# Kernel tuning notes

Measured on AMD Instinct MI355X. Metric: run time of the kernel, lower is better.

## Reference

```python
import jax, jax.numpy as jnp
import numpy as np

B, FRAMES, NBINS, HOP = 4, 400, 129, 240
T = FRAMES * HOP  # 96000


def hann_window(K, dtype=jnp.float32):
    # torch.hann_window default is periodic=True: 0.5*(1 - cos(2*pi*n/K))
    n = jnp.arange(K, dtype=dtype)
    return 0.5 - 0.5 * jnp.cos(2.0 * jnp.pi * n / K)


def get_minimum_phase_fir(log_mag):
    # log_mag: [B, F, NBINS] -> full spectrum [B, F, N], N = 2*(NBINS-1)
    full = jnp.concatenate([log_mag, jnp.flip(log_mag, -1)[..., 1:-1]], axis=-1)
    N = full.shape[-1]
    # Hilbert transform (scipy-style analytic signal), N even
    Xf = jnp.fft.fft(full, axis=-1)
    h = jnp.concatenate([
        jnp.ones((1,), full.dtype),
        2.0 * jnp.ones((N // 2 - 1,), full.dtype),
        jnp.ones((1,), full.dtype),
        jnp.zeros((N // 2 - 1,), full.dtype),
    ])
    analytic = jnp.fft.ifft(Xf * h, axis=-1)
    min_phase = -jnp.imag(analytic)
    freq_resp = jnp.exp(full + 1j * min_phase)
    return jnp.real(jnp.fft.ifft(freq_resp, axis=-1))  # [B, F, N]


def windowing(kernel):
    K = kernel.shape[-1]
    w = hann_window(K, kernel.dtype)
    w = w.at[: K // 2].set(1.0)
    return kernel * w


def upsample_linear(x, scale):
    # x: [B, K, L] -> [B, K, L*scale], matches F.upsample(mode='linear', align_corners=False)
    L = x.shape[-1]
    out = jnp.arange(L * scale, dtype=x.dtype)
    src = jnp.clip((out + 0.5) / scale - 0.5, 0.0, L - 1.0)
    lo = jnp.floor(src).astype(jnp.int32)
    hi = jnp.minimum(lo + 1, L - 1)
    w = src - lo.astype(x.dtype)
    return x[..., lo] * (1.0 - w) + x[..., hi] * w


def fir_filt(x, h):
    # x: [B, T], h: [B, T, K]; causal time-varying FIR: y[t] = sum_k h[t,k] * x[t-k]
    K = h.shape[-1]
    Tn = x.shape[-1]
    x_pad = jnp.pad(x, ((0, 0), (K - 1, 0)))
    idx = jnp.arange(Tn)[:, None] + jnp.arange(K)[None, :]  # [T, K]
    frames = x_pad[:, idx]  # [B, T, K] (im2col-like gather)
    return jnp.einsum('btk,btk->bt', frames, jnp.flip(h, -1))


def setup_inputs() -> dict:
    key = jax.random.key(0)
    k1, k2 = jax.random.split(key)
    ex = jax.random.normal(k1, (B, T), dtype=jnp.float32)
    log_mag = jax.random.normal(k2, (B, FRAMES, NBINS), dtype=jnp.float32)
    return {"ex": ex, "log_mag": log_mag, "hop_length": HOP}


def reference(ex, log_mag, hop_length):
    kernel = get_minimum_phase_fir(log_mag)          # [B, F, K]
    kernel = windowing(kernel)
    up = upsample_linear(jnp.transpose(kernel, (0, 2, 1)), hop_length)  # [B, K, F*hop]
    up = jnp.transpose(up, (0, 2, 1))                # [B, F*hop, K]
    Tn = min(ex.shape[1], up.shape[1])
    ex = ex[:, :Tn]
    up = up[:, :Tn]
    return fir_filt(ex, up)
```

## Files before the change

kernel.cpp:

```cpp
#include <hip/hip_runtime.h>
#include <math.h>

#define NB 4
#define FRAMES 400
#define NBINS 129
#define HOP 240
#define T_LEN (FRAMES * HOP)
#define KLEN 256

#define REC_C { const float cn_ = fmaf(a2, cm, -cm1); cm1 = cm; cm = cn_; }
#define REC_S { const float sn_ = fmaf(a2, sm, -sm1); sm1 = sm; sm = sn_; }

__global__ __launch_bounds__(256) void gen_fir(const float* __restrict__ log_mag,
                                               float* __restrict__ kern) {
    const int bf  = blockIdx.x;
    const int tid = threadIdx.x;
    const int n   = tid & 127;
    const int h   = tid >> 7;

    __shared__ __align__(16) float  full[132];
    __shared__ __align__(16) float  pg[2][128];
    __shared__ __align__(16) float  pm[2][128];
    __shared__ __align__(16) float2 crci[128];
    __shared__ __align__(16) float  pe[2][128];
    __shared__ __align__(16) float  po[2][128];

    const float* lm = log_mag + bf * NBINS;
    if (tid < NBINS) full[tid] = lm[tid];

    const float rev_n = (float)n * (1.0f / 256.0f);
    const float ca = __builtin_amdgcn_cosf(rev_n);
    const float sa = __builtin_amdgcn_sinf(rev_n);
    const float a2  = 2.0f * ca;
    const float sgn = (n & 1) ? -1.0f : 1.0f;

    float cm0, cm1_0, sm0, sm1_0;
    if (h == 0) {
        cm0 = 1.0f;  cm1_0 = ca;
        sm0 = 0.0f;  sm1_0 = -sa;
    } else {
        const float r64 = (float)((64 * n) & 255) * (1.0f / 256.0f);
        const float r63 = (float)((63 * n) & 255) * (1.0f / 256.0f);
        cm0   = __builtin_amdgcn_cosf(r64);
        sm0   = __builtin_amdgcn_sinf(r64);
        cm1_0 = __builtin_amdgcn_cosf(r63);
        sm1_0 = __builtin_amdgcn_sinf(r63);
    }
    __syncthreads();

    const float full0   = full[0];
    const float full128 = full[128];

    {
        const float4* f4p = (const float4*)full;
        float cm1 = cm1_0, cm = cm0, acc = 0.0f;
#pragma unroll 8
        for (int u = 16 * h; u < 16 * h + 16; ++u) {
            const float4 f4 = f4p[u];
            acc = fmaf(f4.x, cm, acc); REC_C;
            acc = fmaf(f4.y, cm, acc); REC_C;
            acc = fmaf(f4.z, cm, acc); REC_C;
            acc = fmaf(f4.w, cm, acc); REC_C;
        }
        const float share = h ? (sgn * full128) : (-full0);
        pg[h][n] = acc * (1.0f / 64.0f) + share * (1.0f / 128.0f);
    }
    __syncthreads();

    {
        const float4* p0 = (const float4*)pg[0];
        const float4* p1 = (const float4*)pg[1];
        float sm1 = sm1_0, sm = sm0, acc = 0.0f;
#pragma unroll 8
        for (int u = 16 * h; u < 16 * h + 16; ++u) {
            const float4 a4 = p0[u];
            const float4 b4 = p1[u];
            acc = fmaf(a4.x + b4.x, sm, acc); REC_S;
            acc = fmaf(a4.y + b4.y, sm, acc); REC_S;
            acc = fmaf(a4.z + b4.z, sm, acc); REC_S;
            acc = fmaf(a4.w + b4.w, sm, acc); REC_S;
        }
        pm[h][n] = acc;
    }
    __syncthreads();

    if (h == 0) {
        const float mp = -(pm[0][n] + pm[1][n]);
        const float e  = __builtin_amdgcn_exp2f(full[n] * 1.4426950408889634f);
        float rev = mp * 0.15915494309189535f;
        rev = rev - floorf(rev);
        const float smp  = __builtin_amdgcn_sinf(rev);
        const float cmp_ = __builtin_amdgcn_cosf(rev);
        const float sc = (n == 0) ? 1.0f : 2.0f;
        crci[n] = make_float2(sc * e * cmp_, sc * e * smp);
    }
    __syncthreads();

    {
        const float4* cc4 = (const float4*)crci;
        float cm1 = cm1_0, cm = cm0;
        float sm1 = sm1_0, sm = sm0;
        float accE = 0.0f, accO = 0.0f;
#pragma unroll 8
        for (int u = 32 * h; u < 32 * h + 32; ++u) {
            const float4 q = cc4[u];
            accE = fmaf(q.x, cm, accE); accE = fmaf(-q.y, sm, accE);
            REC_C; REC_S;
            accO = fmaf(q.z, cm, accO); accO = fmaf(-q.w, sm, accO);
            REC_C; REC_S;
        }
        pe[h][n] = accE;
        po[h][n] = accO;
    }
    __syncthreads();

    if (h == 0) {
        const float accE = pe[0][n] + pe[1][n];
        const float accO = po[0][n] + po[1][n];
        const float e128 = __builtin_amdgcn_exp2f(full128 * 1.4426950408889634f);
        const float base = sgn * e128;
        const float s = 1.0f / 256.0f;
        kern[bf * KLEN + n]       = (accE + accO + base) * s;
        kern[bf * KLEN + n + 128] = (accE - accO + base) * s * (0.5f + 0.5f * ca);
    }
}

__global__ __launch_bounds__(256) void fir_apply(const float* __restrict__ ex,
                                                 const float* __restrict__ kern,
                                                 float* __restrict__ out) {
    const int b   = blockIdx.y;
    const int t0  = blockIdx.x * 512;
    const int tid = threadIdx.x;

    __shared__ __align__(16) float  xs[768];
    __shared__ __align__(16) float2 kp[4][258];

    for (int i = tid; i < 768; i += 256) {
        const int t = t0 - 255 + i;
        xs[i] = (t >= 0 && t < T_LEN) ? ex[b * T_LEN + t] : 0.0f;
    }

    float src0 = ((float)t0 + 0.5f) * (1.0f / HOP) - 0.5f;
    src0 = fminf(fmaxf(src0, 0.0f), (float)(FRAMES - 1));
    const int f0 = (int)src0;
    const float* kb = kern + b * FRAMES * KLEN;
    for (int i = tid; i < 4 * KLEN; i += 256) {
        const int q = i >> 8;
        const int j = i & 255;
        const int fl = min(f0 + q,     FRAMES - 1);
        const int fh = min(f0 + q + 1, FRAMES - 1);
        kp[q][j] = make_float2(kb[fl * KLEN + j], kb[fh * KLEN + j]);
    }
    __syncthreads();

    const int te = t0 + 2 * tid;
    float se = ((float)te + 0.5f) * (1.0f / HOP) - 0.5f;
    se = fminf(fmaxf(se, 0.0f), (float)(FRAMES - 1));
    float so = ((float)te + 1.5f) * (1.0f / HOP) - 0.5f;
    so = fminf(fmaxf(so, 0.0f), (float)(FRAMES - 1));
    const int   lo = (int)se;
    const float we = se - (float)lo;
    const float wo = so - (float)lo;

    const float4* kq4 = (const float4*)&kp[lo - f0][0];

    const int base = 2 * tid;
    float carry = xs[base + 256];
    float aeL = 0.0f, aeH = 0.0f, aoL = 0.0f, aoH = 0.0f;
#pragma unroll 8
    for (int u = 0; u < 128; ++u) {
        const float2 v  = *(const float2*)&xs[base + 254 - 2 * u];
        const float4 k4 = kq4[u];
        aeL = fmaf(v.y,   k4.x, aeL);  aeH = fmaf(v.y,   k4.y, aeH);
        aoL = fmaf(carry, k4.x, aoL);  aoH = fmaf(carry, k4.y, aoH);
        aeL = fmaf(v.x,   k4.z, aeL);  aeH = fmaf(v.x,   k4.w, aeH);
        aoL = fmaf(v.y,   k4.z, aoL);  aoH = fmaf(v.y,   k4.w, aoH);
        carry = v.x;
    }

    if (te < T_LEN)     out[b * T_LEN + te]     = (1.0f - we) * aeL + we * aeH;
    if (te + 1 < T_LEN) out[b * T_LEN + te + 1] = (1.0f - wo) * aoL + wo * aoH;
}

extern "C" void kernel_launch(void* const* d_in, const int* in_sizes, int n_in,
                              void* d_out, int out_size, void* d_ws, size_t ws_size,
                              hipStream_t stream) {
    const float* ex      = (const float*)d_in[0];
    const float* log_mag = (const float*)d_in[1];
    float* kern = (float*)d_ws;
    float* out  = (float*)d_out;

    gen_fir<<<NB * FRAMES, 256, 0, stream>>>(log_mag, kern);

    dim3 grid((T_LEN + 511) / 512, NB);
    fir_apply<<<grid, 256, 0, stream>>>(ex, kern, out);
}
```

Baseline: 24.31 us.

## Fuse FIR generation and filtering into one kernel with per-frame ready flags

Merges the two launches into one grid. The first blocks compute per-frame minimum-phase FIRs and publish a per-row flag. The remaining blocks spin on the flags for the frames they need before loading kernels and filtering. This aims to remove the inter-kernel launch gap and tail, and to overlap filter work with FIR generation. It adds a memset launch, spin-wait overhead, and a forward-progress dependency on generator blocks being scheduled before the consumers that wait on them.

```diff
diff --git a/kernel.cpp b/kernel.cpp
--- a/kernel.cpp
+++ b/kernel.cpp
@@ -7,133 +7,147 @@
 #define HOP 240
 #define T_LEN (FRAMES * HOP)
 #define KLEN 256
+#define NGEN (NB * FRAMES)
+#define NFIRX 188
+#define NFIR (NFIRX * NB)
 
 #define REC_C { const float cn_ = fmaf(a2, cm, -cm1); cm1 = cm; cm = cn_; }
 #define REC_S { const float sn_ = fmaf(a2, sm, -sm1); sm1 = sm; sm = sn_; }
 
-__global__ __launch_bounds__(256) void gen_fir(const float* __restrict__ log_mag,
-                                               float* __restrict__ kern) {
-    const int bf  = blockIdx.x;
+__global__ __launch_bounds__(256) void ltv_fused(const float* __restrict__ ex,
+                                                 const float* __restrict__ log_mag,
+                                                 float* __restrict__ kern,
+                                                 int* __restrict__ flags,
+                                                 float* __restrict__ out) {
+    const int bid = blockIdx.x;
     const int tid = threadIdx.x;
-    const int n   = tid & 127;
-    const int h   = tid >> 7;
-
-    __shared__ __align__(16) float  full[132];
-    __shared__ __align__(16) float  pg[2][128];
-    __shared__ __align__(16) float  pm[2][128];
-    __shared__ __align__(16) float2 crci[128];
-    __shared__ __align__(16) float  pe[2][128];
-    __shared__ __align__(16) float  po[2][128];
-
-    const float* lm = log_mag + bf * NBINS;
-    if (tid < NBINS) full[tid] = lm[tid];
-
-    const float rev_n = (float)n * (1.0f / 256.0f);
-    const float ca = __builtin_amdgcn_cosf(rev_n);
-    const float sa = __builtin_amdgcn_sinf(rev_n);
-    const float a2  = 2.0f * ca;
-    const float sgn = (n & 1) ? -1.0f : 1.0f;
-
-    float cm0, cm1_0, sm0, sm1_0;
-    if (h == 0) {
-        cm0 = 1.0f;  cm1_0 = ca;
-        sm0 = 0.0f;  sm1_0 = -sa;
-    } else {
-        const float r64 = (float)((64 * n) & 255) * (1.0f / 256.0f);
-        const float r63 = (float)((63 * n) & 255) * (1.0f / 256.0f);
-        cm0   = __builtin_amdgcn_cosf(r64);
-        sm0   = __builtin_amdgcn_sinf(r64);
-        cm1_0 = __builtin_amdgcn_cosf(r63);
-        sm1_0 = __builtin_amdgcn_sinf(r63);
-    }
-    __syncthreads();
-
-    const float full0   = full[0];
-    const float full128 = full[128];
-
-    {
-        const float4* f4p = (const float4*)full;
-        float cm1 = cm1_0, cm = cm0, acc = 0.0f;
-#pragma unroll 8
-        for (int u = 16 * h; u < 16 * h + 16; ++u) {
-            const float4 f4 = f4p[u];
-            acc = fmaf(f4.x, cm, acc); REC_C;
-            acc = fmaf(f4.y, cm, acc); REC_C;
-            acc = fmaf(f4.z, cm, acc); REC_C;
-            acc = fmaf(f4.w, cm, acc); REC_C;
-        }
-        const float share = h ? (sgn * full128) : (-full0);
-        pg[h][n] = acc * (1.0f / 64.0f) + share * (1.0f / 128.0f);
-    }
-    __syncthreads();
-
-    {
-        const float4* p0 = (const float4*)pg[0];
-        const float4* p1 = (const float4*)pg[1];
-        float sm1 = sm1_0, sm = sm0, acc = 0.0f;
-#pragma unroll 8
-        for (int u = 16 * h; u < 16 * h + 16; ++u) {
-            const float4 a4 = p0[u];
-            const float4 b4 = p1[u];
-            acc = fmaf(a4.x + b4.x, sm, acc); REC_S;
-            acc = fmaf(a4.y + b4.y, sm, acc); REC_S;
-            acc = fmaf(a4.z + b4.z, sm, acc); REC_S;
-            acc = fmaf(a4.w + b4.w, sm, acc); REC_S;
-        }
-        pm[h][n] = acc;
-    }
-    __syncthreads();
-
-    if (h == 0) {
-        const float mp = -(pm[0][n] + pm[1][n]);
-        const float e  = __builtin_amdgcn_exp2f(full[n] * 1.4426950408889634f);
-        float rev = mp * 0.15915494309189535f;
-        rev = rev - floorf(rev);
-        const float smp  = __builtin_amdgcn_sinf(rev);
-        const float cmp_ = __builtin_amdgcn_cosf(rev);
-        const float sc = (n == 0) ? 1.0f : 2.0f;
-        crci[n] = make_float2(sc * e * cmp_, sc * e * smp);
-    }
-    __syncthreads();
-
-    {
-        const float4* cc4 = (const float4*)crci;
-        float cm1 = cm1_0, cm = cm0;
-        float sm1 = sm1_0, sm = sm0;
-        float accE = 0.0f, accO = 0.0f;
-#pragma unroll 8
-        for (int u = 32 * h; u < 32 * h + 32; ++u) {
-            const float4 q = cc4[u];
-            accE = fmaf(q.x, cm, accE); accE = fmaf(-q.y, sm, accE);
-            REC_C; REC_S;
-            accO = fmaf(q.z, cm, accO); accO = fmaf(-q.w, sm, accO);
-            REC_C; REC_S;
-        }
-        pe[h][n] = accE;
-        po[h][n] = accO;
-    }
-    __syncthreads();
-
-    if (h == 0) {
-        const float accE = pe[0][n] + pe[1][n];
-        const float accO = po[0][n] + po[1][n];
-        const float e128 = __builtin_amdgcn_exp2f(full128 * 1.4426950408889634f);
-        const float base = sgn * e128;
-        const float s = 1.0f / 256.0f;
-        kern[bf * KLEN + n]       = (accE + accO + base) * s;
-        kern[bf * KLEN + n + 128] = (accE - accO + base) * s * (0.5f + 0.5f * ca);
-    }
-}
-
-__global__ __launch_bounds__(256) void fir_apply(const float* __restrict__ ex,
-                                                 const float* __restrict__ kern,
-                                                 float* __restrict__ out) {
-    const int b   = blockIdx.y;
-    const int t0  = blockIdx.x * 512;
-    const int tid = threadIdx.x;
-
-    __shared__ __align__(16) float  xs[768];
-    __shared__ __align__(16) float2 kp[4][258];
+
+    __shared__ __align__(16) float smem[2832];
+
+    if (bid < NGEN) {
+        const int bf = bid;
+        const int n  = tid & 127;
+        const int h  = tid >> 7;
+
+        float*  full = smem;
+        float*  pg0  = smem + 136;
+        float*  pm0  = smem + 392;
+        float2* crci = (float2*)(smem + 648);
+        float*  pe0  = smem + 904;
+        float*  po0  = smem + 1160;
+
+        const float* lm = log_mag + bf * NBINS;
+        if (tid < NBINS) full[tid] = lm[tid];
+
+        const float rev_n = (float)n * (1.0f / 256.0f);
+        const float ca = __builtin_amdgcn_cosf(rev_n);
+        const float sa = __builtin_amdgcn_sinf(rev_n);
+        const float a2  = 2.0f * ca;
+        const float sgn = (n & 1) ? -1.0f : 1.0f;
+
+        float cm0, cm1_0, sm0, sm1_0;
+        if (h == 0) {
+            cm0 = 1.0f;  cm1_0 = ca;
+            sm0 = 0.0f;  sm1_0 = -sa;
+        } else {
+            const float r64 = (float)((64 * n) & 255) * (1.0f / 256.0f);
+            const float r63 = (float)((63 * n) & 255) * (1.0f / 256.0f);
+            cm0   = __builtin_amdgcn_cosf(r64);
+            sm0   = __builtin_amdgcn_sinf(r64);
+            cm1_0 = __builtin_amdgcn_cosf(r63);
+            sm1_0 = __builtin_amdgcn_sinf(r63);
+        }
+        __syncthreads();
+
+        const float full0   = full[0];
+        const float full128 = full[128];
+
+        {
+            const float4* f4p = (const float4*)full;
+            float cm1 = cm1_0, cm = cm0, acc = 0.0f;
+#pragma unroll 8
+            for (int u = 16 * h; u < 16 * h + 16; ++u) {
+                const float4 f4 = f4p[u];
+                acc = fmaf(f4.x, cm, acc); REC_C;
+                acc = fmaf(f4.y, cm, acc); REC_C;
+                acc = fmaf(f4.z, cm, acc); REC_C;
+                acc = fmaf(f4.w, cm, acc); REC_C;
+            }
+            const float share = h ? (sgn * full128) : (-full0);
+            pg0[h * 128 + n] = acc * (1.0f / 64.0f) + share * (1.0f / 128.0f);
+        }
+        __syncthreads();
+
+        {
+            const float4* p0 = (const float4*)pg0;
+            const float4* p1 = (const float4*)(pg0 + 128);
+            float sm1 = sm1_0, sm = sm0, acc = 0.0f;
+#pragma unroll 8
+            for (int u = 16 * h; u < 16 * h + 16; ++u) {
+                const float4 a4 = p0[u];
+                const float4 b4 = p1[u];
+                acc = fmaf(a4.x + b4.x, sm, acc); REC_S;
+                acc = fmaf(a4.y + b4.y, sm, acc); REC_S;
+                acc = fmaf(a4.z + b4.z, sm, acc); REC_S;
+                acc = fmaf(a4.w + b4.w, sm, acc); REC_S;
+            }
+            pm0[h * 128 + n] = acc;
+        }
+        __syncthreads();
+
+        if (h == 0) {
+            const float mp = -(pm0[n] + pm0[128 + n]);
+            const float e  = __builtin_amdgcn_exp2f(full[n] * 1.4426950408889634f);
+            float rev = mp * 0.15915494309189535f;
+            rev = rev - floorf(rev);
+            const float smp  = __builtin_amdgcn_sinf(rev);
+            const float cmp_ = __builtin_amdgcn_cosf(rev);
+            const float sc = (n == 0) ? 1.0f : 2.0f;
+            crci[n] = make_float2(sc * e * cmp_, sc * e * smp);
+        }
+        __syncthreads();
+
+        {
+            const float4* cc4 = (const float4*)crci;
+            float cm1 = cm1_0, cm = cm0;
+            float sm1 = sm1_0, sm = sm0;
+            float accE = 0.0f, accO = 0.0f;
+#pragma unroll 8
+            for (int u = 32 * h; u < 32 * h + 32; ++u) {
+                const float4 q = cc4[u];
+                accE = fmaf(q.x, cm, accE); accE = fmaf(-q.y, sm, accE);
+                REC_C; REC_S;
+                accO = fmaf(q.z, cm, accO); accO = fmaf(-q.w, sm, accO);
+                REC_C; REC_S;
+            }
+            pe0[h * 128 + n] = accE;
+            po0[h * 128 + n] = accO;
+        }
+        __syncthreads();
+
+        if (h == 0) {
+            const float accE = pe0[n] + pe0[128 + n];
+            const float accO = po0[n] + po0[128 + n];
+            const float e128 = __builtin_amdgcn_exp2f(full128 * 1.4426950408889634f);
+            const float base = sgn * e128;
+            const float s = 1.0f / 256.0f;
+            kern[bf * KLEN + n]       = (accE + accO + base) * s;
+            kern[bf * KLEN + n + 128] = (accE - accO + base) * s * (0.5f + 0.5f * ca);
+        }
+        __syncthreads();
+        if (tid == 0) {
+            __threadfence();
+            __hip_atomic_store(&flags[bf], 1, __ATOMIC_RELAXED, __HIP_MEMORY_SCOPE_AGENT);
+        }
+        return;
+    }
+
+    const int idx = bid - NGEN;
+    const int b   = idx / NFIRX;
+    const int t0  = (idx % NFIRX) * 512;
+
+    float*  xs = smem;
+    float2* kp = (float2*)(smem + 768);
 
     for (int i = tid; i < 768; i += 256) {
         const int t = t0 - 255 + i;
@@ -143,13 +157,26 @@
     float src0 = ((float)t0 + 0.5f) * (1.0f / HOP) - 0.5f;
     src0 = fminf(fmaxf(src0, 0.0f), (float)(FRAMES - 1));
     const int f0 = (int)src0;
+
+    if (tid == 0) {
+#pragma unroll
+        for (int d = 0; d < 5; ++d) {
+            const int row = b * FRAMES + min(f0 + d, FRAMES - 1);
+            while (__hip_atomic_load(&flags[row], __ATOMIC_RELAXED,
+                                     __HIP_MEMORY_SCOPE_AGENT) == 0)
+                __builtin_amdgcn_s_sleep(2);
+        }
+        __threadfence();
+    }
+    __syncthreads();
+
     const float* kb = kern + b * FRAMES * KLEN;
     for (int i = tid; i < 4 * KLEN; i += 256) {
         const int q = i >> 8;
         const int j = i & 255;
         const int fl = min(f0 + q,     FRAMES - 1);
         const int fh = min(f0 + q + 1, FRAMES - 1);
-        kp[q][j] = make_float2(kb[fl * KLEN + j], kb[fh * KLEN + j]);
+        kp[q * 258 + j] = make_float2(kb[fl * KLEN + j], kb[fh * KLEN + j]);
     }
     __syncthreads();
 
@@ -162,7 +189,7 @@
     const float we = se - (float)lo;
     const float wo = so - (float)lo;
 
-    const float4* kq4 = (const float4*)&kp[lo - f0][0];
+    const float4* kq4 = (const float4*)&kp[(lo - f0) * 258];
 
     const int base = 2 * tid;
     float carry = xs[base + 256];
@@ -187,11 +214,11 @@
                               hipStream_t stream) {
     const float* ex      = (const float*)d_in[0];
     const float* log_mag = (const float*)d_in[1];
-    float* kern = (float*)d_ws;
-    float* out  = (float*)d_out;
-
-    gen_fir<<<NB * FRAMES, 256, 0, stream>>>(log_mag, kern);
-
-    dim3 grid((T_LEN + 511) / 512, NB);
-    fir_apply<<<grid, 256, 0, stream>>>(ex, kern, out);
+    float* kern  = (float*)d_ws;
+    int*   flags = (int*)((char*)d_ws + NGEN * KLEN * sizeof(float));
+    float* out   = (float*)d_out;
+
+    hipMemsetAsync(flags, 0, NGEN * sizeof(int), stream);
+
+    ltv_fused<<<NGEN + NFIR, 256, 0, stream>>>(ex, log_mag, kern, flags, out);
 }
```

After: 75.50 us. 3.11x slower.
